# Kernel tuning notes

Measured on AMD Instinct MI355X. Metric: run time of the kernel, lower is better.

Reference implementation:

```python
import jax, jax.numpy as jnp
import numpy as np

B, N, DIM = 4, 8192, 512
HEADS, DIM_HEAD = 8, 64
INNER = HEADS * DIM_HEAD


def setup_inputs() -> dict:
    key = jax.random.key(0)
    k1, k2, k3 = jax.random.split(key, 3)
    feats = jax.random.normal(k1, (B, N, DIM), dtype=jnp.float32)
    mask = jnp.ones((B, N), dtype=bool)
    w_qkv = jax.random.normal(k2, (DIM, INNER * 3), dtype=jnp.float32) * 0.02
    w_out = jax.random.normal(k3, (INNER, DIM), dtype=jnp.float32) * 0.02
    b_out = jnp.zeros((DIM,), dtype=jnp.float32)
    return {"feats": feats, "mask": mask, "w_qkv": w_qkv, "w_out": w_out, "b_out": b_out}


def reference(feats, mask, w_qkv, w_out, b_out):
    b, n, _ = feats.shape
    h, d = HEADS, DIM_HEAD
    scale = d ** -0.5

    qkv = feats @ w_qkv                               # [b, n, 3*inner]
    q, k, v = jnp.split(qkv, 3, axis=-1)
    # 'b n (h d) -> b h n d'
    to_heads = lambda t: t.reshape(b, n, h, d).transpose(0, 2, 1, 3)
    q, k, v = to_heads(q), to_heads(k), to_heads(v)

    m = mask[:, None, :, None]                        # 'b n -> b 1 n 1'
    neg = jnp.finfo(k.dtype).max
    k = jnp.where(m, k, -neg)
    v = jnp.where(m, v, 0.0)

    q = jax.nn.softmax(q, axis=-1) * scale            # softmax over d
    k = jax.nn.softmax(k, axis=-2)                    # softmax over n

    context = jnp.einsum('bhnd,bhne->bhde', k, v)     # [b, h, d, d]
    out = jnp.einsum('bhde,bhnd->bhne', context, q)   # [b, h, n, d]
    out = out.transpose(0, 2, 1, 3).reshape(b, n, h * d)
    return out @ w_out + b_out
```

## Files before the change

kernel.cpp:

```cpp
#include <hip/hip_runtime.h>

#define BB 4
#define NN 8192
#define DIM 512
#define HEADS 8
#define INNER 512
#define QKVW 1536
#define BN_ROWS 32768
#define NCHUNK 16
#define CHUNK_ROWS 512

typedef __attribute__((ext_vector_type(8))) short bf16x8;
typedef __attribute__((ext_vector_type(8))) ushort u16x8;
typedef __attribute__((ext_vector_type(4))) float f32x4;

__device__ __forceinline__ ushort f2b(float x) {
  unsigned u = __float_as_uint(x);
  u = (u + 0x7FFFu + ((u >> 16) & 1u)) >> 16;
  return (ushort)u;
}
__device__ __forceinline__ float b2f(ushort u) {
  return __uint_as_float((unsigned)u << 16);
}

__device__ __forceinline__ void gload16(const ushort* src, ushort* lds) {
  __builtin_amdgcn_global_load_lds(
      (const __attribute__((address_space(1))) void*)src,
      (__attribute__((address_space(3))) void*)lds, 16, 0, 0);
}

#define BAR() __builtin_amdgcn_s_barrier()
#define LGKM0() do { asm volatile("s_waitcnt lgkmcnt(0)" ::: "memory"); \
                     __builtin_amdgcn_sched_barrier(0); } while (0)
#define VMC4() asm volatile("s_waitcnt vmcnt(4)" ::: "memory")

template<int MODE>
__global__ __launch_bounds__(512, 2) void gemm_nt_bf16(
    const ushort* __restrict__ A, const ushort* __restrict__ BT,
    void* __restrict__ Cv, const float* __restrict__ bias,
    int K, int lda, int ldb, int ldc, long sA, long sB, long sC)
{
  const int gx = gridDim.x;
  const int nwg = gx * gridDim.y;
  const int hid = blockIdx.y * gx + blockIdx.x;
  const int lid = (hid & 7) * (nwg >> 3) + (hid >> 3);
  const int bx = lid % gx, by = lid / gx;

  const int bz = blockIdx.z;
  const long row0 = (long)by * 256;
  const int col0 = bx * 256;
  const ushort* Ag = A + (long)bz * sA + row0 * (long)lda;
  const ushort* Bg = BT + (long)bz * sB + (long)col0 * ldb;
  ushort* Cb = (ushort*)Cv + (long)bz * sC;
  float*  Cf = (float*)Cv + (long)bz * sC;

  __shared__ alignas(16) ushort As[2][256 * 64];
  __shared__ alignas(16) ushort Bs[2][256 * 64];

  const int tid = threadIdx.x;
  const int lane = tid & 63, wv = tid >> 6;
  const int wm = wv >> 2, wn = wv & 3;
  const int l15 = lane & 15, l4 = lane >> 4;

  auto stageA = [&](int buf, int half, int kt) {
#pragma unroll
    for (int i = 0; i < 2; i++) {
      int ci = i * 512 + tid;
      int r = ci >> 3, p = ci & 7;
      gload16(Ag + (long)(half * 128 + r) * lda + kt * 64 + ((p ^ (r & 7)) << 3),
              &As[buf][half * 8192 + ci * 8]);
    }
  };
  auto stageB = [&](int buf, int half, int kt) {
#pragma unroll
    for (int i = 0; i < 2; i++) {
      int ci = i * 512 + tid;
      int r = ci >> 3, p = ci & 7;
      gload16(Bg + (long)(half * 128 + r) * ldb + kt * 64 + ((p ^ (r & 7)) << 3),
              &Bs[buf][half * 8192 + ci * 8]);
    }
  };
  auto rdA = [&](int buf, int mi, int s) {
    int rr = wm * 128 + mi * 16 + l15;
    return *(const bf16x8*)(&As[buf][rr * 64 + (((4 * s + l4) ^ (rr & 7)) << 3)]);
  };
  auto rdB = [&](int buf, int ni, int s) {
    int rr = wn * 64 + ni * 16 + l15;
    return *(const bf16x8*)(&Bs[buf][rr * 64 + (((4 * s + l4) ^ (rr & 7)) << 3)]);
  };

  bf16x8 af[4][2], bfr[4][2];
  f32x4 acc[8][4] = {};

  auto mfmaQ = [&](int mh, int nh) {
    __builtin_amdgcn_s_setprio(1);
#pragma unroll
    for (int mi = 0; mi < 4; mi++)
#pragma unroll
      for (int ni = 0; ni < 2; ni++)
#pragma unroll
        for (int s = 0; s < 2; s++)
          acc[mh * 4 + mi][nh * 2 + ni] = __builtin_amdgcn_mfma_f32_16x16x32_bf16(
              af[mi][s], bfr[nh * 2 + ni][s], acc[mh * 4 + mi][nh * 2 + ni], 0, 0, 0);
    __builtin_amdgcn_s_setprio(0);
  };

  stageA(0, 0, 0); stageA(0, 1, 0); stageB(0, 0, 0); stageB(0, 1, 0);
  stageB(1, 0, 1); stageB(1, 1, 1);
  VMC4(); BAR();

  const int NT = K >> 6;
  for (int j = 0; j < (NT >> 1); j++) {
    const int Te = 2 * j, To = 2 * j + 1;
#pragma unroll
    for (int mi = 0; mi < 4; mi++) { af[mi][0] = rdA(0, mi, 0); af[mi][1] = rdA(0, mi, 1); }
#pragma unroll
    for (int ni = 0; ni < 2; ni++) { bfr[ni][0] = rdB(0, ni, 0); bfr[ni][1] = rdB(0, ni, 1); }
    stageA(1, 0, To);
    BAR(); LGKM0(); mfmaQ(0, 0); BAR();
#pragma unroll
    for (int ni = 2; ni < 4; ni++) { bfr[ni][0] = rdB(0, ni, 0); bfr[ni][1] = rdB(0, ni, 1); }
    stageA(1, 1, To);
    BAR(); LGKM0(); mfmaQ(0, 1); BAR();
#pragma unroll
    for (int mi = 0; mi < 4; mi++) { af[mi][0] = rdA(0, mi + 4, 0); af[mi][1] = rdA(0, mi + 4, 1); }
    if (Te + 2 < NT) stageB(0, 0, Te + 2);
    BAR(); LGKM0(); mfmaQ(1, 1); BAR();
    if (Te + 2 < NT) stageB(0, 1, Te + 2);
    BAR(); mfmaQ(1, 0); VMC4(); BAR();
#pragma unroll
    for (int mi = 0; mi < 4; mi++) { af[mi][0] = rdA(1, mi, 0); af[mi][1] = rdA(1, mi, 1); }
#pragma unroll
    for (int ni = 0; ni < 2; ni++) { bfr[ni][0] = rdB(1, ni, 0); bfr[ni][1] = rdB(1, ni, 1); }
    if (Te + 2 < NT) stageA(0, 0, Te + 2);
    BAR(); LGKM0(); mfmaQ(0, 0); BAR();
#pragma unroll
    for (int ni = 2; ni < 4; ni++) { bfr[ni][0] = rdB(1, ni, 0); bfr[ni][1] = rdB(1, ni, 1); }
    if (Te + 2 < NT) stageA(0, 1, Te + 2);
    BAR(); LGKM0(); mfmaQ(0, 1); BAR();
#pragma unroll
    for (int mi = 0; mi < 4; mi++) { af[mi][0] = rdA(1, mi + 4, 0); af[mi][1] = rdA(1, mi + 4, 1); }
    if (To + 2 < NT) stageB(1, 0, To + 2);
    BAR(); LGKM0(); mfmaQ(1, 1); BAR();
    if (To + 2 < NT) stageB(1, 1, To + 2);
    BAR(); mfmaQ(1, 0); VMC4(); BAR();
  }

  const int colg0 = col0 + wn * 64;
  const long rowg0 = row0 + wm * 128;

  if constexpr (MODE == 0) {
#pragma unroll
    for (int mi = 0; mi < 8; mi++)
#pragma unroll
      for (int ni = 0; ni < 4; ni++) {
        int cc = colg0 + ni * 16 + l15;
        float bv = bias[cc];
#pragma unroll
        for (int e = 0; e < 4; e++) {
          long rr = rowg0 + mi * 16 + l4 * 4 + e;
          Cf[rr * (long)ldc + cc] = acc[mi][ni][e] + bv;
        }
      }
  } else {
    const int sect = bx >> 1;
    if (sect == 0) {
#pragma unroll
      for (int mi = 0; mi < 8; mi++) {
        float ex[4][4];
        float s[4] = {0.f, 0.f, 0.f, 0.f};
#pragma unroll
        for (int ni = 0; ni < 4; ni++)
#pragma unroll
          for (int e = 0; e < 4; e++) {
            ex[ni][e] = __expf(acc[mi][ni][e]);
            s[e] += ex[ni][e];
          }
#pragma unroll
        for (int e = 0; e < 4; e++) {
          float t = s[e];
#pragma unroll
          for (int off = 1; off <= 8; off <<= 1) t += __shfl_xor(t, off);
          s[e] = 0.125f / t;
        }
#pragma unroll
        for (int ni = 0; ni < 4; ni++) {
          int cc = colg0 + ni * 16 + l15;
#pragma unroll
          for (int e = 0; e < 4; e++) {
            long rr = rowg0 + mi * 16 + l4 * 4 + e;
            Cb[rr * (long)ldc + cc] = f2b(ex[ni][e] * s[e]);
          }
        }
      }
    } else {
#pragma unroll
      for (int mi = 0; mi < 8; mi++)
#pragma unroll
        for (int ni = 0; ni < 4; ni++) {
          int cc = colg0 + ni * 16 + l15;
#pragma unroll
          for (int e = 0; e < 4; e++) {
            long rr = rowg0 + mi * 16 + l4 * 4 + e;
            float v = acc[mi][ni][e];
            Cb[rr * (long)ldc + cc] = f2b(sect == 1 ? __expf(v) : v);
          }
        }
    }
  }
}

__global__ __launch_bounds__(256) void cvt_f32_bf16(const float* __restrict__ in,
                                                    ushort* __restrict__ out)
{
  long i = ((long)blockIdx.x * 256 + threadIdx.x) * 8;
  float4 a = *(const float4*)(in + i);
  float4 b = *(const float4*)(in + i + 4);
  u16x8 o;
  o[0] = f2b(a.x); o[1] = f2b(a.y); o[2] = f2b(a.z); o[3] = f2b(a.w);
  o[4] = f2b(b.x); o[5] = f2b(b.y); o[6] = f2b(b.z); o[7] = f2b(b.w);
  *(u16x8*)(out + i) = o;
}

__global__ __launch_bounds__(256) void cvt_wqkvT(const float* __restrict__ in,
                                                 ushort* __restrict__ out)
{
  int idx = blockIdx.x * 256 + threadIdx.x;
  int n = idx >> 9, k = idx & 511;
  out[idx] = f2b(in[(long)k * QKVW + n]);
}

__global__ __launch_bounds__(256) void ctx_partial_kernel(
    const ushort* __restrict__ qkv,
    float* __restrict__ ctx_p, float* __restrict__ den_p)
{
  const int bh = blockIdx.y, chunk = blockIdx.x;
  const int b = bh >> 3, h = bh & 7;
  const ushort* ekb = qkv + (long)b * NN * QKVW + INNER + h * 64;
  const ushort* vb = ekb + INNER;
  const int tid = threadIdx.x;
  const int ds = tid & 63, rs = tid >> 6;

  __shared__ float ek[32][64];
  __shared__ float vv[32][64];
  __shared__ float dred[4][64];

  float den = 0.f;
  const int tx = tid & 15, ty = tid >> 4;
  float acc[4][4] = {};
  const int nbase = chunk * CHUNK_ROWS;

  for (int n0 = 0; n0 < CHUNK_ROWS; n0 += 32) {
    __syncthreads();
#pragma unroll
    for (int i = 0; i < 8; i++) {
      int r = rs * 8 + i;
      long off = (long)(nbase + n0 + r) * QKVW + ds;
      float e = b2f(ekb[off]);
      ek[r][ds] = e;
      den += e;
      vv[r][ds] = b2f(vb[off]);
    }
    __syncthreads();
#pragma unroll
    for (int kk = 0; kk < 32; kk++) {
      float4 a = *(float4*)&ek[kk][ty * 4];
      float4 bb = *(float4*)&vv[kk][tx * 4];
      float av[4] = {a.x, a.y, a.z, a.w};
      float bvv[4] = {bb.x, bb.y, bb.z, bb.w};
#pragma unroll
      for (int i = 0; i < 4; i++)
#pragma unroll
        for (int j = 0; j < 4; j++)
          acc[i][j] = fmaf(av[i], bvv[j], acc[i][j]);
    }
  }

  __syncthreads();
  dred[rs][ds] = den;
  __syncthreads();
  if (rs == 0)
    den_p[(bh * NCHUNK + chunk) * 64 + ds] =
        dred[0][ds] + dred[1][ds] + dred[2][ds] + dred[3][ds];

  float* cp = ctx_p + (long)(bh * NCHUNK + chunk) * 4096;
#pragma unroll
  for (int i = 0; i < 4; i++) {
    float4 o = make_float4(acc[i][0], acc[i][1], acc[i][2], acc[i][3]);
    *(float4*)&cp[(ty * 4 + i) * 64 + tx * 4] = o;
  }
}

__global__ __launch_bounds__(256) void ctx_reduce_kernel(
    const float* __restrict__ ctx_p, const float* __restrict__ den_p,
    float* __restrict__ ctx)
{
  const int bh = blockIdx.x;
  const int tid = threadIdx.x;
  __shared__ float den[64];
  if (tid < 64) {
    float s = 0.f;
    for (int c = 0; c < NCHUNK; c++) s += den_p[(bh * NCHUNK + c) * 64 + tid];
    den[tid] = s;
  }
  __syncthreads();
  for (int i = tid; i < 4096; i += 256) {
    int d = i >> 6;
    float s = 0.f;
    for (int c = 0; c < NCHUNK; c++) s += ctx_p[(long)(bh * NCHUNK + c) * 4096 + i];
    ctx[(long)bh * 4096 + i] = s / den[d];
  }
}

__global__ __launch_bounds__(256) void w2_kernel(
    const float* __restrict__ ctx, const float* __restrict__ w_out,
    ushort* __restrict__ W2T)
{
  const int bh = blockIdx.y, jc = blockIdx.x;
  const int b = bh >> 3, h = bh & 7;
  __shared__ float cs[64][65];
  for (int i = threadIdx.x; i < 4096; i += 256)
    cs[i >> 6][i & 63] = ctx[(long)bh * 4096 + i];
  __syncthreads();
  const int tx = threadIdx.x & 31, ty = threadIdx.x >> 5;
  float acc[8][4] = {};
  for (int e = 0; e < 64; e++) {
    float4 w = *(const float4*)&w_out[(long)(h * 64 + e) * DIM + jc * 128 + tx * 4];
#pragma unroll
    for (int i = 0; i < 8; i++) {
      float a = cs[ty * 8 + i][e];
      acc[i][0] = fmaf(a, w.x, acc[i][0]);
      acc[i][1] = fmaf(a, w.y, acc[i][1]);
      acc[i][2] = fmaf(a, w.z, acc[i][2]);
      acc[i][3] = fmaf(a, w.w, acc[i][3]);
    }
  }
#pragma unroll
  for (int i = 0; i < 8; i++)
#pragma unroll
    for (int q = 0; q < 4; q++) {
      int j = jc * 128 + tx * 4 + q;
      int k = h * 64 + ty * 8 + i;
      W2T[((long)b * DIM + j) * DIM + k] = f2b(acc[i][q]);
    }
}

extern "C" void kernel_launch(void* const* d_in, const int* in_sizes, int n_in,
                              void* d_out, int out_size, void* d_ws, size_t ws_size,
                              hipStream_t stream)
{
  const float* feats = (const float*)d_in[0];
  const float* w_qkv = (const float*)d_in[2];
  const float* w_out = (const float*)d_in[3];
  const float* b_out = (const float*)d_in[4];
  float* out = (float*)d_out;

  ushort* qkv = (ushort*)d_ws;
  ushort* feb = qkv + (long)BN_ROWS * QKVW;
  ushort* wqT = feb + (long)BN_ROWS * DIM;
  ushort* w2t = wqT + (long)QKVW * DIM;
  float* ctx_p  = (float*)(w2t + (long)BB * DIM * DIM);
  float* den_p  = ctx_p + (long)32 * NCHUNK * 4096;
  float* ctx    = den_p + 32 * NCHUNK * 64;

  cvt_f32_bf16<<<dim3((BN_ROWS * DIM) / (256 * 8)), 256, 0, stream>>>(feats, feb);
  cvt_wqkvT<<<dim3((QKVW * DIM) / 256), 256, 0, stream>>>(w_qkv, wqT);

  gemm_nt_bf16<1><<<dim3(QKVW / 256, BN_ROWS / 256, 1), 512, 0, stream>>>(
      feb, wqT, qkv, nullptr, DIM, DIM, DIM, QKVW, 0, 0, 0);

  ctx_partial_kernel<<<dim3(NCHUNK, 32), 256, 0, stream>>>(qkv, ctx_p, den_p);

  ctx_reduce_kernel<<<dim3(32), 256, 0, stream>>>(ctx_p, den_p, ctx);

  w2_kernel<<<dim3(4, 32), 256, 0, stream>>>(ctx, w_out, w2t);

  gemm_nt_bf16<0><<<dim3(DIM / 256, NN / 256, BB), 512, 0, stream>>>(
      qkv, w2t, out, b_out, DIM, QKVW, DIM, DIM,
      (long)NN * QKVW, (long)DIM * DIM, (long)NN * DIM);
}
```

Baseline: 174.6 us.

## Write exp(K) and V transposed from QKV GEMM and compute context with MFMA

The QKV GEMM epilogue now stages the exp(K) and V tiles through shared memory and writes them transposed (d-major, n contiguous) into separate buffers, while Q goes to a compact buffer. The context kernel is replaced with an MFMA bf16 kernel that reads these transposed tiles with async LDS loads, in place of scalar fp32 FMAs over strided rows. This trades an extra LDS round-trip in the GEMM epilogue for much cheaper context accumulation and a narrower A operand stride in the output GEMM. A vmcnt(0) wait on the last iteration is added so all loads have landed before shared memory is reused.

New measurement: 160.0 us. -8.3%, faster.

```diff
diff --git a/kernel.cpp b/kernel.cpp
--- a/kernel.cpp
+++ b/kernel.cpp
@@ -7,8 +7,7 @@
 #define INNER 512
 #define QKVW 1536
 #define BN_ROWS 32768
-#define NCHUNK 16
-#define CHUNK_ROWS 512
+#define KC 16
 
 typedef __attribute__((ext_vector_type(8))) short bf16x8;
 typedef __attribute__((ext_vector_type(8))) ushort u16x8;
@@ -33,11 +32,13 @@
 #define LGKM0() do { asm volatile("s_waitcnt lgkmcnt(0)" ::: "memory"); \
                      __builtin_amdgcn_sched_barrier(0); } while (0)
 #define VMC4() asm volatile("s_waitcnt vmcnt(4)" ::: "memory")
+#define VMC0() asm volatile("s_waitcnt vmcnt(0)" ::: "memory")
 
 template<int MODE>
 __global__ __launch_bounds__(512, 2) void gemm_nt_bf16(
     const ushort* __restrict__ A, const ushort* __restrict__ BT,
     void* __restrict__ Cv, const float* __restrict__ bias,
+    ushort* __restrict__ T1, ushort* __restrict__ T2,
     int K, int lda, int ldb, int ldc, long sA, long sB, long sC)
 {
   const int gx = gridDim.x;
@@ -54,8 +55,9 @@
   ushort* Cb = (ushort*)Cv + (long)bz * sC;
   float*  Cf = (float*)Cv + (long)bz * sC;
 
-  __shared__ alignas(16) ushort As[2][256 * 64];
-  __shared__ alignas(16) ushort Bs[2][256 * 64];
+  __shared__ alignas(16) ushort smem[65536];
+  auto Asb = [&](int buf) { return smem + buf * 16384; };
+  auto Bsb = [&](int buf) { return smem + 32768 + buf * 16384; };
 
   const int tid = threadIdx.x;
   const int lane = tid & 63, wv = tid >> 6;
@@ -68,7 +70,7 @@
       int ci = i * 512 + tid;
       int r = ci >> 3, p = ci & 7;
       gload16(Ag + (long)(half * 128 + r) * lda + kt * 64 + ((p ^ (r & 7)) << 3),
-              &As[buf][half * 8192 + ci * 8]);
+              Asb(buf) + half * 8192 + ci * 8);
     }
   };
   auto stageB = [&](int buf, int half, int kt) {
@@ -77,16 +79,16 @@
       int ci = i * 512 + tid;
       int r = ci >> 3, p = ci & 7;
       gload16(Bg + (long)(half * 128 + r) * ldb + kt * 64 + ((p ^ (r & 7)) << 3),
-              &Bs[buf][half * 8192 + ci * 8]);
+              Bsb(buf) + half * 8192 + ci * 8);
     }
   };
   auto rdA = [&](int buf, int mi, int s) {
     int rr = wm * 128 + mi * 16 + l15;
-    return *(const bf16x8*)(&As[buf][rr * 64 + (((4 * s + l4) ^ (rr & 7)) << 3)]);
+    return *(const bf16x8*)(Asb(buf) + rr * 64 + (((4 * s + l4) ^ (rr & 7)) << 3));
   };
   auto rdB = [&](int buf, int ni, int s) {
     int rr = wn * 64 + ni * 16 + l15;
-    return *(const bf16x8*)(&Bs[buf][rr * 64 + (((4 * s + l4) ^ (rr & 7)) << 3)]);
+    return *(const bf16x8*)(Bsb(buf) + rr * 64 + (((4 * s + l4) ^ (rr & 7)) << 3));
   };
 
   bf16x8 af[4][2], bfr[4][2];
@@ -112,6 +114,7 @@
   const int NT = K >> 6;
   for (int j = 0; j < (NT >> 1); j++) {
     const int Te = 2 * j, To = 2 * j + 1;
+    const bool more = (Te + 2) < NT;
 #pragma unroll
     for (int mi = 0; mi < 4; mi++) { af[mi][0] = rdA(0, mi, 0); af[mi][1] = rdA(0, mi, 1); }
 #pragma unroll
@@ -124,19 +127,21 @@
     BAR(); LGKM0(); mfmaQ(0, 1); BAR();
 #pragma unroll
     for (int mi = 0; mi < 4; mi++) { af[mi][0] = rdA(0, mi + 4, 0); af[mi][1] = rdA(0, mi + 4, 1); }
-    if (Te + 2 < NT) stageB(0, 0, Te + 2);
+    if (more) stageB(0, 0, Te + 2);
     BAR(); LGKM0(); mfmaQ(1, 1); BAR();
-    if (Te + 2 < NT) stageB(0, 1, Te + 2);
-    BAR(); mfmaQ(1, 0); VMC4(); BAR();
+    if (more) stageB(0, 1, Te + 2);
+    BAR(); mfmaQ(1, 0);
+    if (more) VMC4(); else VMC0();
+    BAR();
 #pragma unroll
     for (int mi = 0; mi < 4; mi++) { af[mi][0] = rdA(1, mi, 0); af[mi][1] = rdA(1, mi, 1); }
 #pragma unroll
     for (int ni = 0; ni < 2; ni++) { bfr[ni][0] = rdB(1, ni, 0); bfr[ni][1] = rdB(1, ni, 1); }
-    if (Te + 2 < NT) stageA(0, 0, Te + 2);
+    if (more) stageA(0, 0, Te + 2);
     BAR(); LGKM0(); mfmaQ(0, 0); BAR();
 #pragma unroll
     for (int ni = 2; ni < 4; ni++) { bfr[ni][0] = rdB(1, ni, 0); bfr[ni][1] = rdB(1, ni, 1); }
-    if (Te + 2 < NT) stageA(0, 1, Te + 2);
+    if (more) stageA(0, 1, Te + 2);
     BAR(); LGKM0(); mfmaQ(0, 1); BAR();
 #pragma unroll
     for (int mi = 0; mi < 4; mi++) { af[mi][0] = rdA(1, mi + 4, 0); af[mi][1] = rdA(1, mi + 4, 1); }
@@ -198,14 +203,28 @@
       for (int mi = 0; mi < 8; mi++)
 #pragma unroll
         for (int ni = 0; ni < 4; ni++) {
-          int cc = colg0 + ni * 16 + l15;
-#pragma unroll
-          for (int e = 0; e < 4; e++) {
-            long rr = rowg0 + mi * 16 + l4 * 4 + e;
-            float v = acc[mi][ni][e];
-            Cb[rr * (long)ldc + cc] = f2b(sect == 1 ? __expf(v) : v);
-          }
+          int c_loc = wn * 64 + ni * 16 + l15;
+          int rbase = wm * 128 + mi * 16 + l4 * 4;
+          ushort4 pk;
+          float v0 = acc[mi][ni][0], v1 = acc[mi][ni][1];
+          float v2 = acc[mi][ni][2], v3 = acc[mi][ni][3];
+          if (sect == 1) { v0 = __expf(v0); v1 = __expf(v1); v2 = __expf(v2); v3 = __expf(v3); }
+          pk.x = f2b(v0); pk.y = f2b(v1); pk.z = f2b(v2); pk.w = f2b(v3);
+          int chunk = (rbase >> 3) ^ (c_loc & 31);
+          *(ushort4*)&smem[c_loc * 256 + (chunk << 3) + (rbase & 7)] = pk;
         }
+      __syncthreads();
+      ushort* Tdst = (sect == 1) ? T1 : T2;
+      const int c = tid >> 1, hf = tid & 1;
+      const int dg0 = col0 - sect * 512;
+      const int bb = (int)(row0 >> 13);
+      const long nb = row0 & 8191;
+      ushort* dst = Tdst + ((long)bb * 512 + dg0 + c) * 8192 + nb + hf * 128;
+#pragma unroll
+      for (int jj = 0; jj < 16; jj++) {
+        int phys = (hf * 16 + jj) ^ (c & 31);
+        *(u16x8*)(dst + jj * 8) = *(const u16x8*)&smem[c * 256 + phys * 8];
+      }
     }
   }
 }
@@ -230,65 +249,97 @@
   out[idx] = f2b(in[(long)k * QKVW + n]);
 }
 
-__global__ __launch_bounds__(256) void ctx_partial_kernel(
-    const ushort* __restrict__ qkv,
+__global__ __launch_bounds__(256) void ctx_mfma_kernel(
+    const ushort* __restrict__ ekT, const ushort* __restrict__ vT,
     float* __restrict__ ctx_p, float* __restrict__ den_p)
 {
-  const int bh = blockIdx.y, chunk = blockIdx.x;
+  const int bh = blockIdx.y, kc = blockIdx.x;
   const int b = bh >> 3, h = bh & 7;
-  const ushort* ekb = qkv + (long)b * NN * QKVW + INNER + h * 64;
-  const ushort* vb = ekb + INNER;
-  const int tid = threadIdx.x;
-  const int ds = tid & 63, rs = tid >> 6;
-
-  __shared__ float ek[32][64];
-  __shared__ float vv[32][64];
-  __shared__ float dred[4][64];
-
-  float den = 0.f;
-  const int tx = tid & 15, ty = tid >> 4;
-  float acc[4][4] = {};
-  const int nbase = chunk * CHUNK_ROWS;
-
-  for (int n0 = 0; n0 < CHUNK_ROWS; n0 += 32) {
+  const long base = ((long)b * 512 + h * 64) * 8192 + kc * (NN / KC);
+  const ushort* Ae = ekT + base;
+  const ushort* Vv = vT + base;
+
+  __shared__ alignas(16) ushort Asm[64 * 64];
+  __shared__ alignas(16) ushort Bsm[64 * 64];
+
+  const int tid = threadIdx.x, lane = tid & 63, wv = tid >> 6;
+  const int wr = wv >> 1, wc = wv & 1;
+  const int l15 = lane & 15, l4 = lane >> 4;
+
+  f32x4 acc[2][2] = {};
+  float dacc[2] = {0.f, 0.f};
+
+  for (int k0 = 0; k0 < NN / KC; k0 += 64) {
     __syncthreads();
 #pragma unroll
-    for (int i = 0; i < 8; i++) {
-      int r = rs * 8 + i;
-      long off = (long)(nbase + n0 + r) * QKVW + ds;
-      float e = b2f(ekb[off]);
-      ek[r][ds] = e;
-      den += e;
-      vv[r][ds] = b2f(vb[off]);
+    for (int i = 0; i < 2; i++) {
+      int ci = i * 256 + tid;
+      int r = ci >> 3, p = ci & 7;
+      gload16(Ae + (long)r * 8192 + k0 + ((p ^ (r & 7)) << 3), &Asm[ci * 8]);
+    }
+#pragma unroll
+    for (int i = 0; i < 2; i++) {
+      int ci = i * 256 + tid;
+      int r = ci >> 3, p = ci & 7;
+      gload16(Vv + (long)r * 8192 + k0 + ((p ^ (r & 7)) << 3), &Bsm[ci * 8]);
     }
     __syncthreads();
-#pragma unroll
-    for (int kk = 0; kk < 32; kk++) {
-      float4 a = *(float4*)&ek[kk][ty * 4];
-      float4 bb = *(float4*)&vv[kk][tx * 4];
-      float av[4] = {a.x, a.y, a.z, a.w};
-      float bvv[4] = {bb.x, bb.y, bb.z, bb.w};
-#pragma unroll
-      for (int i = 0; i < 4; i++)
-#pragma unroll
-        for (int j = 0; j < 4; j++)
-          acc[i][j] = fmaf(av[i], bvv[j], acc[i][j]);
-    }
-  }
-
-  __syncthreads();
-  dred[rs][ds] = den;
-  __syncthreads();
-  if (rs == 0)
-    den_p[(bh * NCHUNK + chunk) * 64 + ds] =
-        dred[0][ds] + dred[1][ds] + dred[2][ds] + dred[3][ds];
-
-  float* cp = ctx_p + (long)(bh * NCHUNK + chunk) * 4096;
-#pragma unroll
-  for (int i = 0; i < 4; i++) {
-    float4 o = make_float4(acc[i][0], acc[i][1], acc[i][2], acc[i][3]);
-    *(float4*)&cp[(ty * 4 + i) * 64 + tx * 4] = o;
-  }
+
+    bf16x8 af[2][2], bfr[2][2];
+#pragma unroll
+    for (int mi = 0; mi < 2; mi++)
+#pragma unroll
+      for (int s = 0; s < 2; s++) {
+        int r = wr * 32 + mi * 16 + l15;
+        af[mi][s] = *(const bf16x8*)&Asm[r * 64 + (((s * 4 + l4) ^ (r & 7)) << 3)];
+      }
+#pragma unroll
+    for (int ni = 0; ni < 2; ni++)
+#pragma unroll
+      for (int s = 0; s < 2; s++) {
+        int r = wc * 32 + ni * 16 + l15;
+        bfr[ni][s] = *(const bf16x8*)&Bsm[r * 64 + (((s * 4 + l4) ^ (r & 7)) << 3)];
+      }
+#pragma unroll
+    for (int mi = 0; mi < 2; mi++)
+#pragma unroll
+      for (int ni = 0; ni < 2; ni++)
+#pragma unroll
+        for (int s = 0; s < 2; s++)
+          acc[mi][ni] = __builtin_amdgcn_mfma_f32_16x16x32_bf16(
+              af[mi][s], bfr[ni][s], acc[mi][ni], 0, 0, 0);
+    if (wc == 0) {
+#pragma unroll
+      for (int mi = 0; mi < 2; mi++)
+#pragma unroll
+        for (int s = 0; s < 2; s++) {
+          float t = 0.f;
+#pragma unroll
+          for (int e = 0; e < 8; e++) t += b2f((ushort)af[mi][s][e]);
+          dacc[mi] += t;
+        }
+    }
+  }
+
+  if (wc == 0) {
+#pragma unroll
+    for (int mi = 0; mi < 2; mi++) {
+      float t = dacc[mi];
+      t += __shfl_xor(t, 16);
+      t += __shfl_xor(t, 32);
+      if (l4 == 0)
+        den_p[(bh * KC + kc) * 64 + wr * 32 + mi * 16 + l15] = t;
+    }
+  }
+
+  float* cp = ctx_p + ((long)bh * KC + kc) * 4096;
+#pragma unroll
+  for (int mi = 0; mi < 2; mi++)
+#pragma unroll
+    for (int ni = 0; ni < 2; ni++)
+#pragma unroll
+      for (int e = 0; e < 4; e++)
+        cp[(wr * 32 + mi * 16 + l4 * 4 + e) * 64 + wc * 32 + ni * 16 + l15] = acc[mi][ni][e];
 }
 
 __global__ __launch_bounds__(256) void ctx_reduce_kernel(
@@ -300,14 +351,14 @@
   __shared__ float den[64];
   if (tid < 64) {
     float s = 0.f;
-    for (int c = 0; c < NCHUNK; c++) s += den_p[(bh * NCHUNK + c) * 64 + tid];
+    for (int c = 0; c < KC; c++) s += den_p[(bh * KC + c) * 64 + tid];
     den[tid] = s;
   }
   __syncthreads();
   for (int i = tid; i < 4096; i += 256) {
     int d = i >> 6;
     float s = 0.f;
-    for (int c = 0; c < NCHUNK; c++) s += ctx_p[(long)(bh * NCHUNK + c) * 4096 + i];
+    for (int c = 0; c < KC; c++) s += ctx_p[(long)(bh * KC + c) * 4096 + i];
     ctx[(long)bh * 4096 + i] = s / den[d];
   }
 }
@@ -355,27 +406,29 @@
   const float* b_out = (const float*)d_in[4];
   float* out = (float*)d_out;
 
-  ushort* qkv = (ushort*)d_ws;
-  ushort* feb = qkv + (long)BN_ROWS * QKVW;
+  ushort* qsm = (ushort*)d_ws;
+  ushort* ekT = qsm + (long)BN_ROWS * DIM;
+  ushort* vT  = ekT + (long)BB * DIM * NN;
+  ushort* feb = vT + (long)BB * DIM * NN;
   ushort* wqT = feb + (long)BN_ROWS * DIM;
   ushort* w2t = wqT + (long)QKVW * DIM;
   float* ctx_p  = (float*)(w2t + (long)BB * DIM * DIM);
-  float* den_p  = ctx_p + (long)32 * NCHUNK * 4096;
-  float* ctx    = den_p + 32 * NCHUNK * 64;
+  float* den_p  = ctx_p + (long)32 * KC * 4096;
+  float* ctx    = den_p + 32 * KC * 64;
 
   cvt_f32_bf16<<<dim3((BN_ROWS * DIM) / (256 * 8)), 256, 0, stream>>>(feats, feb);
   cvt_wqkvT<<<dim3((QKVW * DIM) / 256), 256, 0, stream>>>(w_qkv, wqT);
 
   gemm_nt_bf16<1><<<dim3(QKVW / 256, BN_ROWS / 256, 1), 512, 0, stream>>>(
-      feb, wqT, qkv, nullptr, DIM, DIM, DIM, QKVW, 0, 0, 0);
-
-  ctx_partial_kernel<<<dim3(NCHUNK, 32), 256, 0, stream>>>(qkv, ctx_p, den_p);
+      feb, wqT, qsm, nullptr, ekT, vT, DIM, DIM, DIM, 512, 0, 0, 0);
+
+  ctx_mfma_kernel<<<dim3(KC, 32), 256, 0, stream>>>(ekT, vT, ctx_p, den_p);
 
   ctx_reduce_kernel<<<dim3(32), 256, 0, stream>>>(ctx_p, den_p, ctx);
 
   w2_kernel<<<dim3(4, 32), 256, 0, stream>>>(ctx, w_out, w2t);
 
   gemm_nt_bf16<0><<<dim3(DIM / 256, NN / 256, BB), 512, 0, stream>>>(
-      qkv, w2t, out, b_out, DIM, QKVW, DIM, DIM,
-      (long)NN * QKVW, (long)DIM * DIM, (long)NN * DIM);
-}
+      qsm, w2t, out, b_out, nullptr, nullptr, DIM, DIM, DIM, DIM,
+      (long)NN * DIM, (long)DIM * DIM, (long)NN * DIM);
+}
```
